# Kernel optimization log

Measured on AMD Instinct MI355X. Metric: run time of the kernel, lower is better.

## Reference

```python
import jax, jax.numpy as jnp
import numpy as np

N_NODES = 100000
N_EDGES = 800000
F_IN = 128
HID = 128
HEADS = 4
HEAD_DIM = HID // HEADS
LAYERS = 3
N_CLASSES = 40
NEG_SLOPE = 0.2
BN_EPS = 1e-5


def setup_inputs() -> dict:
    key = jax.random.key(0)
    ks = jax.random.split(key, 10)
    feat = jax.random.normal(ks[0], (N_NODES, F_IN), dtype=jnp.float32)
    src = jax.random.randint(ks[1], (N_EDGES,), 0, N_NODES, dtype=jnp.int32)
    dst = jax.random.randint(ks[2], (N_EDGES,), 0, N_NODES, dtype=jnp.int32)
    W_enc = jax.random.normal(ks[3], (F_IN, HID), dtype=jnp.float32) / np.sqrt(F_IN)
    b_enc = jnp.zeros((HID,), dtype=jnp.float32)
    Ws = jax.random.normal(ks[4], (LAYERS, HID, HID), dtype=jnp.float32) / np.sqrt(HID)
    attn_ls = jax.random.normal(ks[5], (LAYERS, HEADS, HEAD_DIM), dtype=jnp.float32) / np.sqrt(HEAD_DIM)
    attn_rs = jax.random.normal(ks[6], (LAYERS, HEADS, HEAD_DIM), dtype=jnp.float32) / np.sqrt(HEAD_DIM)
    biases = jnp.zeros((LAYERS, HID), dtype=jnp.float32)
    gammas = jnp.ones((LAYERS, HID), dtype=jnp.float32)
    betas = jnp.zeros((LAYERS, HID), dtype=jnp.float32)
    W_pred = jax.random.normal(ks[7], (HID, N_CLASSES), dtype=jnp.float32) / np.sqrt(HID)
    b_pred = jnp.zeros((N_CLASSES,), dtype=jnp.float32)
    return {"feat": feat, "src": src, "dst": dst, "W_enc": W_enc, "b_enc": b_enc,
            "Ws": Ws, "attn_ls": attn_ls, "attn_rs": attn_rs, "biases": biases,
            "gammas": gammas, "betas": betas, "W_pred": W_pred, "b_pred": b_pred}


def _gat_layer(h, src, dst, W, a_l, a_r, bias, n_nodes):
    # h: [N, HID] -> projected per-head features [N, H, D]
    hf = (h @ W).reshape(n_nodes, HEADS, HEAD_DIM)
    el = jnp.sum(hf * a_l, axis=-1)  # [N, H]
    er = jnp.sum(hf * a_r, axis=-1)  # [N, H]
    e = jax.nn.leaky_relu(el[src] + er[dst], NEG_SLOPE)  # [E, H]
    # edge softmax over incoming edges of each destination node
    m = jax.ops.segment_max(e, dst, num_segments=n_nodes)  # [N, H]
    ex = jnp.exp(e - m[dst])
    s = jax.ops.segment_sum(ex, dst, num_segments=n_nodes)  # [N, H]
    alpha = ex / s[dst]  # [E, H]
    msg = hf[src] * alpha[:, :, None]  # [E, H, D]
    out = jax.ops.segment_sum(msg, dst, num_segments=n_nodes)  # [N, H, D]
    return out.reshape(n_nodes, HEADS * HEAD_DIM) + bias


def _batchnorm(x, gamma, beta):
    mean = jnp.mean(x, axis=0)
    var = jnp.var(x, axis=0)
    return gamma * (x - mean) * jax.lax.rsqrt(var + BN_EPS) + beta


def reference(feat, src, dst, W_enc, b_enc, Ws, attn_ls, attn_rs, biases, gammas, betas, W_pred, b_pred):
    n_nodes = feat.shape[0]
    h = jax.nn.relu(feat @ W_enc + b_enc)
    h_last = None
    for i in range(Ws.shape[0]):
        h = _gat_layer(h, src, dst, Ws[i], attn_ls[i], attn_rs[i], biases[i], n_nodes)
        if h_last is not None:
            h = h + h_last
        h_last = h
        h = _batchnorm(h, gammas[i], betas[i])
        h = jax.nn.relu(h)
    return h @ W_pred + b_pred
```

## Files before the change

kernel.cpp:

```cpp
#include <hip/hip_runtime.h>

typedef __attribute__((ext_vector_type(8))) short short8;
typedef __attribute__((ext_vector_type(4))) float f32x4;

#define N_NODES 100000
#define N_EDGES 800000
#define NEG 0.2f
#define BN_EPS 1e-5f
#define AGG_GRID 2048

__device__ __forceinline__ ushort bf16b(float f) {
  unsigned u = __float_as_uint(f);
  return (ushort)((u + 0x7FFFu + ((u >> 16) & 1u)) >> 16);
}
__device__ __forceinline__ float bflo(unsigned u) { return __uint_as_float(u << 16); }
__device__ __forceinline__ float bfhi(unsigned u) { return __uint_as_float(u & 0xFFFF0000u); }

__global__ void k_hist(const int* __restrict__ dst, int* __restrict__ cnt, int e) {
  int i = blockIdx.x * blockDim.x + threadIdx.x;
  if (i < e) atomicAdd(&cnt[dst[i]], 1);
}

__global__ void k_scan1(const int* __restrict__ cnt, int* __restrict__ rowptr,
                        int* __restrict__ bsums, int n) {
  __shared__ int sm[256];
  int i = blockIdx.x * 256 + threadIdx.x;
  int v = (i < n) ? cnt[i] : 0;
  sm[threadIdx.x] = v;
  __syncthreads();
  for (int off = 1; off < 256; off <<= 1) {
    int t = (threadIdx.x >= off) ? sm[threadIdx.x - off] : 0;
    __syncthreads();
    sm[threadIdx.x] += t;
    __syncthreads();
  }
  if (i < n) rowptr[i + 1] = sm[threadIdx.x];
  if (threadIdx.x == 255) bsums[blockIdx.x] = sm[255];
}

__global__ void k_scan2(int* __restrict__ bsums, int nb) {
  __shared__ int sm[512];
  int v = (threadIdx.x < nb) ? bsums[threadIdx.x] : 0;
  sm[threadIdx.x] = v;
  __syncthreads();
  for (int off = 1; off < 512; off <<= 1) {
    int t = (threadIdx.x >= off) ? sm[threadIdx.x - off] : 0;
    __syncthreads();
    sm[threadIdx.x] += t;
    __syncthreads();
  }
  if (threadIdx.x < nb) bsums[threadIdx.x] = sm[threadIdx.x] - v;
}

__global__ void k_scan3(int* __restrict__ rowptr, const int* __restrict__ bsums,
                        int* __restrict__ cursor, int n) {
  int i = blockIdx.x * 256 + threadIdx.x;
  if (i < n) {
    int val = rowptr[i + 1] + bsums[blockIdx.x];
    rowptr[i + 1] = val;
    if (i + 1 < n) cursor[i + 1] = val;
  }
  if (i == 0) { rowptr[0] = 0; cursor[0] = 0; }
}

__global__ void k_scatter(const int* __restrict__ src, const int* __restrict__ dst,
                          int* __restrict__ cursor, int* __restrict__ ssort,
                          int* __restrict__ dsort, int e) {
  int i = blockIdx.x * blockDim.x + threadIdx.x;
  if (i < e) {
    int d = dst[i];
    int pos = atomicAdd(&cursor[d], 1);
    ssort[pos] = src[i];
    dsort[pos] = d;
  }
}

__global__ void k_packW(const float* __restrict__ W_enc, const float* __restrict__ Ws,
                        ushort* __restrict__ Wp) {
  int s = blockIdx.x * 256 + threadIdx.x;
  int wi = s >> 11, s2 = s & 2047;
  int kt = s2 >> 9, nb8 = (s2 >> 6) & 7, l = s2 & 63;
  const float* Wsrc = (wi == 0) ? W_enc : Ws + (size_t)(wi - 1) * 16384;
  int n = nb8 * 16 + (l & 15);
  int k0 = kt * 32 + (l >> 4) * 8;
  unsigned pk[4];
#pragma unroll
  for (int j = 0; j < 4; ++j) {
    ushort lo = bf16b(Wsrc[(size_t)(k0 + 2 * j) * 128 + n]);
    ushort hi = bf16b(Wsrc[(size_t)(k0 + 2 * j + 1) * 128 + n]);
    pk[j] = (unsigned)lo | ((unsigned)hi << 16);
  }
  *(uint4*)&Wp[(size_t)s * 8] = make_uint4(pk[0], pk[1], pk[2], pk[3]);
}

template <int MODE>
__global__ __launch_bounds__(256) void k_mgemm(
    const float* __restrict__ Af, const ushort* __restrict__ Ab,
    const ushort* __restrict__ Wp, const float* __restrict__ bias,
    const float* __restrict__ stats, const float* __restrict__ al,
    const float* __restrict__ ar, float* __restrict__ el, float* __restrict__ er,
    ushort* __restrict__ Cb) {
  __shared__ __align__(16) ushort Al[32 * 128];
  int tid = threadIdx.x;
  int lane = tid & 63, w = tid >> 6;
  int wr = w & 1, wc = w >> 1;
  int l15 = lane & 15, l4 = lane >> 4;
  int rb = blockIdx.x * 32;

  const uint4* wp4 = (const uint4*)Wp;
  short8 bfr[4][4];
#pragma unroll
  for (int kt = 0; kt < 4; ++kt) {
#pragma unroll
    for (int nb = 0; nb < 4; ++nb) {
      uint4 t = wp4[(size_t)((kt * 8 + wc * 4 + nb) * 64 + lane)];
      bfr[kt][nb] = *(short8*)&t;
    }
  }

  {
    int row = tid >> 3;
    int c16 = (tid & 7) * 16;
    int kc0 = (tid & 7) * 2;
    char* base = (char*)Al + row * 256;
    if (MODE == 1) {
      const uint4* srcp = (const uint4*)(Ab + (size_t)(rb + row) * 128 + c16);
      uint4 v0 = srcp[0], v1 = srcp[1];
      *(uint4*)(base + ((kc0 ^ (row & 7)) << 4)) = v0;
      *(uint4*)(base + (((kc0 + 1) ^ (row & 7)) << 4)) = v1;
    } else {
      const float4* srcp = (const float4*)(Af + (size_t)(rb + row) * 128 + c16);
      float4 f[4];
#pragma unroll
      for (int j = 0; j < 4; ++j) f[j] = srcp[j];
      if (MODE == 2) {
#pragma unroll
        for (int j = 0; j < 4; ++j) {
          float4 sc = *(const float4*)&stats[c16 + 4 * j];
          float4 sh = *(const float4*)&stats[128 + c16 + 4 * j];
          f[j].x = fmaxf(f[j].x * sc.x + sh.x, 0.f);
          f[j].y = fmaxf(f[j].y * sc.y + sh.y, 0.f);
          f[j].z = fmaxf(f[j].z * sc.z + sh.z, 0.f);
          f[j].w = fmaxf(f[j].w * sc.w + sh.w, 0.f);
        }
      }
      unsigned pk[8];
#pragma unroll
      for (int j = 0; j < 4; ++j) {
        pk[2 * j] = (unsigned)bf16b(f[j].x) | ((unsigned)bf16b(f[j].y) << 16);
        pk[2 * j + 1] = (unsigned)bf16b(f[j].z) | ((unsigned)bf16b(f[j].w) << 16);
      }
      *(uint4*)(base + ((kc0 ^ (row & 7)) << 4)) = make_uint4(pk[0], pk[1], pk[2], pk[3]);
      *(uint4*)(base + (((kc0 + 1) ^ (row & 7)) << 4)) = make_uint4(pk[4], pk[5], pk[6], pk[7]);
    }
  }
  __syncthreads();

  f32x4 acc[4];
#pragma unroll
  for (int nb = 0; nb < 4; ++nb) acc[nb] = (f32x4){0.f, 0.f, 0.f, 0.f};
  int arow = 16 * wr + l15;
  const char* abase = (const char*)Al + arow * 256;
  int sw = arow & 7;
#pragma unroll
  for (int kt = 0; kt < 4; ++kt) {
    short8 af = *(const short8*)(abase + (((kt * 4 + l4) ^ sw) << 4));
    acc[0] = __builtin_amdgcn_mfma_f32_16x16x32_bf16(af, bfr[kt][0], acc[0], 0, 0, 0);
    acc[1] = __builtin_amdgcn_mfma_f32_16x16x32_bf16(af, bfr[kt][1], acc[1], 0, 0, 0);
    acc[2] = __builtin_amdgcn_mfma_f32_16x16x32_bf16(af, bfr[kt][2], acc[2], 0, 0, 0);
    acc[3] = __builtin_amdgcn_mfma_f32_16x16x32_bf16(af, bfr[kt][3], acc[3], 0, 0, 0);
  }

  float alv0 = 0, alv1 = 0, alv2 = 0, alv3 = 0;
  float arv0 = 0, arv1 = 0, arv2 = 0, arv3 = 0;
  float bv0 = 0, bv1 = 0, bv2 = 0, bv3 = 0;
  if (MODE != 0) {
    alv0 = al[64 * wc + l15];      arv0 = ar[64 * wc + l15];
    alv1 = al[64 * wc + 16 + l15]; arv1 = ar[64 * wc + 16 + l15];
    alv2 = al[64 * wc + 32 + l15]; arv2 = ar[64 * wc + 32 + l15];
    alv3 = al[64 * wc + 48 + l15]; arv3 = ar[64 * wc + 48 + l15];
  } else {
    bv0 = bias[64 * wc + l15];      bv1 = bias[64 * wc + 16 + l15];
    bv2 = bias[64 * wc + 32 + l15]; bv3 = bias[64 * wc + 48 + l15];
  }
  int row0 = rb + 16 * wr + 4 * l4;
#pragma unroll
  for (int i = 0; i < 4; ++i) {
    int row = row0 + i;
    if (MODE != 0) {
      float pl0 = acc[0][i] * alv0 + acc[1][i] * alv1;
      float pr0 = acc[0][i] * arv0 + acc[1][i] * arv1;
      float pl1 = acc[2][i] * alv2 + acc[3][i] * alv3;
      float pr1 = acc[2][i] * arv2 + acc[3][i] * arv3;
#pragma unroll
      for (int o = 1; o < 16; o <<= 1) {
        pl0 += __shfl_xor(pl0, o); pr0 += __shfl_xor(pr0, o);
        pl1 += __shfl_xor(pl1, o); pr1 += __shfl_xor(pr1, o);
      }
      if (l15 == 0) {
        el[(size_t)row * 4 + 2 * wc] = pl0;     er[(size_t)row * 4 + 2 * wc] = pr0;
        el[(size_t)row * 4 + 2 * wc + 1] = pl1; er[(size_t)row * 4 + 2 * wc + 1] = pr1;
      }
    }
    float v0 = acc[0][i], v1 = acc[1][i], v2 = acc[2][i], v3 = acc[3][i];
    if (MODE == 0) {
      v0 = fmaxf(v0 + bv0, 0.f); v1 = fmaxf(v1 + bv1, 0.f);
      v2 = fmaxf(v2 + bv2, 0.f); v3 = fmaxf(v3 + bv3, 0.f);
    }
    size_t rbase = (size_t)row * 128 + 64 * wc + l15;
    Cb[rbase] = bf16b(v0);
    Cb[rbase + 16] = bf16b(v1);
    Cb[rbase + 32] = bf16b(v2);
    Cb[rbase + 48] = bf16b(v3);
  }
}

__global__ __launch_bounds__(256) void k_elmax1(const float* __restrict__ el,
                                                float4* __restrict__ part, int n) {
  int gid = blockIdx.x * 256 + threadIdx.x;
  float4 m = make_float4(-1e30f, -1e30f, -1e30f, -1e30f);
  for (int i = gid; i < n; i += 128 * 256) {
    float4 v = *(const float4*)&el[(size_t)4 * i];
    m.x = fmaxf(m.x, v.x); m.y = fmaxf(m.y, v.y);
    m.z = fmaxf(m.z, v.z); m.w = fmaxf(m.w, v.w);
  }
  __shared__ float4 sm[256];
  sm[threadIdx.x] = m;
  __syncthreads();
  for (int off = 128; off; off >>= 1) {
    if (threadIdx.x < off) {
      float4 o = sm[threadIdx.x + off];
      sm[threadIdx.x].x = fmaxf(sm[threadIdx.x].x, o.x);
      sm[threadIdx.x].y = fmaxf(sm[threadIdx.x].y, o.y);
      sm[threadIdx.x].z = fmaxf(sm[threadIdx.x].z, o.z);
      sm[threadIdx.x].w = fmaxf(sm[threadIdx.x].w, o.w);
    }
    __syncthreads();
  }
  if (threadIdx.x == 0) part[blockIdx.x] = sm[0];
}

__global__ void k_elmax2(const float4* __restrict__ part, float* __restrict__ elmax) {
  __shared__ float4 sm[128];
  int t = threadIdx.x;
  sm[t] = part[t];
  __syncthreads();
  for (int off = 64; off; off >>= 1) {
    if (t < off) {
      float4 o = sm[t + off];
      sm[t].x = fmaxf(sm[t].x, o.x);
      sm[t].y = fmaxf(sm[t].y, o.y);
      sm[t].z = fmaxf(sm[t].z, o.z);
      sm[t].w = fmaxf(sm[t].w, o.w);
    }
    __syncthreads();
  }
  if (t == 0) {
    elmax[0] = sm[0].x; elmax[1] = sm[0].y;
    elmax[2] = sm[0].z; elmax[3] = sm[0].w;
  }
}

__global__ __launch_bounds__(256) void k_edgew(
    const int* __restrict__ ssort, const int* __restrict__ dsort,
    const float* __restrict__ el, const float* __restrict__ er,
    const float* __restrict__ elmax, float4* __restrict__ wgt, int e) {
  int j = blockIdx.x * 256 + threadIdx.x;
  if (j >= e) return;
  int s = ssort[j], d = dsort[j];
  float4 elv = *(const float4*)&el[(size_t)4 * s];
  float4 erv = *(const float4*)&er[(size_t)4 * d];
  float m0 = elmax[0] + erv.x;
  float m1 = elmax[1] + erv.y;
  float m2 = elmax[2] + erv.z;
  float m3 = elmax[3] + erv.w;
  m0 = fmaxf(m0, NEG * m0); m1 = fmaxf(m1, NEG * m1);
  m2 = fmaxf(m2, NEG * m2); m3 = fmaxf(m3, NEG * m3);
  float e0 = elv.x + erv.x; e0 = fmaxf(e0, NEG * e0);
  float e1 = elv.y + erv.y; e1 = fmaxf(e1, NEG * e1);
  float e2 = elv.z + erv.z; e2 = fmaxf(e2, NEG * e2);
  float e3 = elv.w + erv.w; e3 = fmaxf(e3, NEG * e3);
  float4 wv;
  wv.x = __expf(e0 - m0); wv.y = __expf(e1 - m1);
  wv.z = __expf(e2 - m2); wv.w = __expf(e3 - m3);
  wgt[j] = wv;
}

__global__ __launch_bounds__(256, 8) void k_aggregate(
    const ushort* __restrict__ hf, const float4* __restrict__ wgt,
    const int* __restrict__ rowptr, const int* __restrict__ ssort,
    const float* __restrict__ bias, float* __restrict__ hpre,
    float* __restrict__ part, int n, int addres) {
  int tid = threadIdx.x;
  int w = tid >> 6, lane = tid & 63;
  int h = lane >> 4;
  int c0 = 2 * lane;
  float2 bb = *(const float2*)&bias[c0];
  float sbn0 = 0.f, sbn1 = 0.f, qbn0 = 0.f, qbn1 = 0.f;
  for (int wid = blockIdx.x * 4 + w; wid < n; wid += AGG_GRID * 4) {
    int beg = rowptr[wid], end = rowptr[wid + 1];
    float s0 = 0.f, a00 = 0.f, a10 = 0.f;
    float s1 = 0.f, a01 = 0.f, a11 = 0.f;
    float s2 = 0.f, a02 = 0.f, a12 = 0.f;
    float s3 = 0.f, a03 = 0.f, a13 = 0.f;
    int j = beg;
    int rem = (end - beg) & 3;
    for (int t = 0; t < rem; ++t, ++j) {
      int sA = ssort[j];
      float wA = ((const float*)(wgt + j))[h];
      unsigned hA = *(const unsigned*)(hf + (size_t)sA * 128 + c0);
      s0 += wA; a00 += wA * bflo(hA); a10 += wA * bfhi(hA);
    }
    for (; j < end; j += 4) {
      int sA = ssort[j], sB = ssort[j + 1], sC = ssort[j + 2], sD = ssort[j + 3];
      float wA = ((const float*)(wgt + j))[h];
      float wB = ((const float*)(wgt + j + 1))[h];
      float wC = ((const float*)(wgt + j + 2))[h];
      float wD = ((const float*)(wgt + j + 3))[h];
      unsigned hA = *(const unsigned*)(hf + (size_t)sA * 128 + c0);
      unsigned hB = *(const unsigned*)(hf + (size_t)sB * 128 + c0);
      unsigned hC = *(const unsigned*)(hf + (size_t)sC * 128 + c0);
      unsigned hD = *(const unsigned*)(hf + (size_t)sD * 128 + c0);
      s0 += wA; a00 += wA * bflo(hA); a10 += wA * bfhi(hA);
      s1 += wB; a01 += wB * bflo(hB); a11 += wB * bfhi(hB);
      s2 += wC; a02 += wC * bflo(hC); a12 += wC * bfhi(hC);
      s3 += wD; a03 += wD * bflo(hD); a13 += wD * bfhi(hD);
    }
    float s = (s0 + s1) + (s2 + s3);
    float inv = (end > beg) ? 1.f / s : 0.f;
    float a0 = ((a00 + a01) + (a02 + a03)) * inv;
    float a1 = ((a10 + a11) + (a12 + a13)) * inv;
    float r0 = 0.f, r1 = 0.f;
    if (addres) {
      float2 rr = *(const float2*)(hpre + (size_t)wid * 128 + c0);
      r0 = rr.x; r1 = rr.y;
    }
    float o0 = a0 + bb.x + r0, o1 = a1 + bb.y + r1;
    *(float2*)(hpre + (size_t)wid * 128 + c0) = make_float2(o0, o1);
    sbn0 += o0; qbn0 += o0 * o0;
    sbn1 += o1; qbn1 += o1 * o1;
  }
  __shared__ float red_s[4][128];
  __shared__ float red_q[4][128];
  red_s[w][c0] = sbn0; red_s[w][c0 + 1] = sbn1;
  red_q[w][c0] = qbn0; red_q[w][c0 + 1] = qbn1;
  __syncthreads();
  if (tid < 128)
    part[(size_t)blockIdx.x * 256 + tid] =
        (red_s[0][tid] + red_s[1][tid]) + (red_s[2][tid] + red_s[3][tid]);
  else if (tid < 256) {
    int c = tid - 128;
    part[(size_t)blockIdx.x * 256 + tid] =
        (red_q[0][c] + red_q[1][c]) + (red_q[2][c] + red_q[3][c]);
  }
}

__global__ __launch_bounds__(320) void k_pred(
    const float* __restrict__ A, const float* __restrict__ stats,
    const float* __restrict__ W, const float* __restrict__ bias,
    float* __restrict__ out, int n) {
  __shared__ float Wl[128 * 40];
  __shared__ float Xl[32 * 132];
  for (int i = threadIdx.x; i < 128 * 40; i += 320) Wl[i] = W[i];
  int cg = threadIdx.x % 10;
  int rg = threadIdx.x / 10;
  float4 bv = *(const float4*)&bias[4 * cg];
  for (int rb = blockIdx.x * 32; rb < n; rb += gridDim.x * 32) {
    __syncthreads();
    for (int idx = threadIdx.x; idx < 1024; idx += 320) {
      int r = idx >> 5, c = (idx & 31) * 4;
      float4 v = *(const float4*)&A[(size_t)(rb + r) * 128 + c];
      float4 sc = *(const float4*)&stats[c];
      float4 sh = *(const float4*)&stats[128 + c];
      v.x = fmaxf(v.x * sc.x + sh.x, 0.f);
      v.y = fmaxf(v.y * sc.y + sh.y, 0.f);
      v.z = fmaxf(v.z * sc.z + sh.z, 0.f);
      v.w = fmaxf(v.w * sc.w + sh.w, 0.f);
      *(float4*)&Xl[r * 132 + c] = v;
    }
    __syncthreads();
    float a0 = 0.f, a1 = 0.f, a2 = 0.f, a3 = 0.f;
#pragma unroll 4
    for (int k = 0; k < 128; ++k) {
      float x = Xl[rg * 132 + k];
      float4 w = *(float4*)&Wl[k * 40 + 4 * cg];
      a0 += x * w.x; a1 += x * w.y; a2 += x * w.z; a3 += x * w.w;
    }
    float4 o = make_float4(a0 + bv.x, a1 + bv.y, a2 + bv.z, a3 + bv.w);
    *(float4*)&out[(size_t)(rb + rg) * 40 + 4 * cg] = o;
  }
}

__global__ __launch_bounds__(256) void k_bnred(const float* __restrict__ part,
                                               float* __restrict__ colsum, int g) {
  int v = blockIdx.x;
  float acc = 0.f;
  for (int b = threadIdx.x; b < g; b += 256) acc += part[(size_t)b * 256 + v];
  __shared__ float sm[256];
  sm[threadIdx.x] = acc;
  __syncthreads();
  for (int off = 128; off; off >>= 1) {
    if (threadIdx.x < off) sm[threadIdx.x] += sm[threadIdx.x + off];
    __syncthreads();
  }
  if (threadIdx.x == 0) colsum[v] = sm[0];
}

__global__ void k_bnstat(const float* __restrict__ colsum, const float* __restrict__ gamma,
                         const float* __restrict__ beta, float* __restrict__ stats, int n) {
  int c = threadIdx.x;
  float mean = colsum[c] / n;
  float var = colsum[128 + c] / n - mean * mean;
  float rstd = rsqrtf(var + BN_EPS);
  float scale = gamma[c] * rstd;
  stats[c] = scale;
  stats[128 + c] = beta[c] - mean * scale;
}

extern "C" void kernel_launch(void* const* d_in, const int* in_sizes, int n_in,
                              void* d_out, int out_size, void* d_ws, size_t ws_size,
                              hipStream_t stream) {
  const float* feat   = (const float*)d_in[0];
  const int*   src    = (const int*)d_in[1];
  const int*   dst    = (const int*)d_in[2];
  const float* W_enc  = (const float*)d_in[3];
  const float* b_enc  = (const float*)d_in[4];
  const float* Ws     = (const float*)d_in[5];
  const float* a_ls   = (const float*)d_in[6];
  const float* a_rs   = (const float*)d_in[7];
  const float* biases = (const float*)d_in[8];
  const float* gammas = (const float*)d_in[9];
  const float* betas  = (const float*)d_in[10];
  const float* W_pred = (const float*)d_in[11];
  const float* b_pred = (const float*)d_in[12];
  float* out = (float*)d_out;

  char* p = (char*)d_ws;
  auto alloc = [&](size_t bytes) {
    char* q = p;
    p += (bytes + 255) & ~(size_t)255;
    return q;
  };
  ushort* h_bf  = (ushort*)alloc((size_t)N_NODES * 128 * 2);
  ushort* hf_bf = (ushort*)alloc((size_t)N_NODES * 128 * 2);
  float* hpre   = (float*)alloc((size_t)N_NODES * 128 * 4);
  float* el     = (float*)alloc((size_t)N_NODES * 4 * 4);
  float* er     = (float*)alloc((size_t)N_NODES * 4 * 4);
  float* part   = (float*)alloc((size_t)AGG_GRID * 256 * 4);
  float* colsum = (float*)alloc(256 * 4);
  float* stats  = (float*)alloc(256 * 4);
  ushort* Wpack = (ushort*)alloc((size_t)4 * 2048 * 16);
  float4* elpart= (float4*)alloc(128 * 16);
  float* elmax  = (float*)alloc(4 * 4);
  int* rowptr   = (int*)alloc((size_t)(N_NODES + 1) * 4);
  int* cursor   = (int*)alloc((size_t)N_NODES * 4);
  int* bsums    = (int*)alloc(512 * 4);
  int* ssort    = (int*)alloc((size_t)N_EDGES * 4);
  int* dsort    = (int*)alloc((size_t)N_EDGES * 4);
  float4* wgt   = (float4*)alloc((size_t)N_EDGES * 16);

  hipMemsetAsync(cursor, 0, (size_t)N_NODES * 4, stream);
  k_hist<<<(N_EDGES + 255) / 256, 256, 0, stream>>>(dst, cursor, N_EDGES);
  int nb = (N_NODES + 255) / 256;
  k_scan1<<<nb, 256, 0, stream>>>(cursor, rowptr, bsums, N_NODES);
  k_scan2<<<1, 512, 0, stream>>>(bsums, nb);
  k_scan3<<<nb, 256, 0, stream>>>(rowptr, bsums, cursor, N_NODES);
  k_scatter<<<(N_EDGES + 255) / 256, 256, 0, stream>>>(src, dst, cursor, ssort, dsort,
                                                       N_EDGES);

  k_packW<<<32, 256, 0, stream>>>(W_enc, Ws, Wpack);

  k_mgemm<0><<<3125, 256, 0, stream>>>(feat, nullptr, Wpack, b_enc, nullptr, nullptr,
                                       nullptr, nullptr, nullptr, h_bf);

  for (int L = 0; L < 3; ++L) {
    const float* al = a_ls + L * 128;
    const float* ar = a_rs + L * 128;
    const ushort* wp = Wpack + (size_t)(1 + L) * 16384;
    if (L == 0)
      k_mgemm<1><<<3125, 256, 0, stream>>>(nullptr, h_bf, wp, nullptr, nullptr, al, ar,
                                           el, er, hf_bf);
    else
      k_mgemm<2><<<3125, 256, 0, stream>>>(hpre, nullptr, wp, nullptr, stats, al, ar,
                                           el, er, hf_bf);
    k_elmax1<<<128, 256, 0, stream>>>(el, elpart, N_NODES);
    k_elmax2<<<1, 128, 0, stream>>>(elpart, elmax);
    k_edgew<<<(N_EDGES + 255) / 256, 256, 0, stream>>>(ssort, dsort, el, er, elmax,
                                                       wgt, N_EDGES);
    k_aggregate<<<AGG_GRID, 256, 0, stream>>>(hf_bf, wgt, rowptr, ssort,
                                              biases + L * 128, hpre, part, N_NODES,
                                              L > 0 ? 1 : 0);
    k_bnred<<<256, 256, 0, stream>>>(part, colsum, AGG_GRID);
    k_bnstat<<<1, 128, 0, stream>>>(colsum, gammas + L * 128, betas + L * 128, stats,
                                    N_NODES);
  }
  k_pred<<<1563, 320, 0, stream>>>(hpre, stats, W_pred, b_pred, out, N_NODES);
}
```

Measured before the change: 432.2 us.

## Store layer pre-activations in bf16 and interleave sorted src/dst indices

The per-layer aggregated output hpre (residual and BN input) is now stored as bf16 instead of fp32, which halves its read/write traffic in the aggregate, GEMM-prologue and prediction kernels. The sorted source and destination arrays are merged into one int2 array, so edge-weight computation issues a single load per edge. The cost is that the aggregate kernel now loads 8 bytes per edge where it only needs 4, and the residual path loses precision because it is accumulated from bf16 values across layers.

Result: faster. 419.2 us (-3.0%).

```diff
diff --git a/kernel.cpp b/kernel.cpp
--- a/kernel.cpp
+++ b/kernel.cpp
@@ -64,14 +64,12 @@
 }
 
 __global__ void k_scatter(const int* __restrict__ src, const int* __restrict__ dst,
-                          int* __restrict__ cursor, int* __restrict__ ssort,
-                          int* __restrict__ dsort, int e) {
+                          int* __restrict__ cursor, int2* __restrict__ esort, int e) {
   int i = blockIdx.x * blockDim.x + threadIdx.x;
   if (i < e) {
     int d = dst[i];
     int pos = atomicAdd(&cursor[d], 1);
-    ssort[pos] = src[i];
-    dsort[pos] = d;
+    esort[pos] = make_int2(src[i], d);
   }
 }
 
@@ -128,22 +126,35 @@
       uint4 v0 = srcp[0], v1 = srcp[1];
       *(uint4*)(base + ((kc0 ^ (row & 7)) << 4)) = v0;
       *(uint4*)(base + (((kc0 + 1) ^ (row & 7)) << 4)) = v1;
+    } else if (MODE == 2) {
+      const uint4* srcp = (const uint4*)(Ab + (size_t)(rb + row) * 128 + c16);
+      uint4 v0 = srcp[0], v1 = srcp[1];
+      unsigned pk[8];
+#pragma unroll
+      for (int j = 0; j < 4; ++j) {
+        unsigned wv = ((const unsigned*)&v0)[j];
+        float2 sc = *(const float2*)&stats[c16 + 2 * j];
+        float2 sh = *(const float2*)&stats[128 + c16 + 2 * j];
+        float x0 = fmaxf(bflo(wv) * sc.x + sh.x, 0.f);
+        float x1 = fmaxf(bfhi(wv) * sc.y + sh.y, 0.f);
+        pk[j] = (unsigned)bf16b(x0) | ((unsigned)bf16b(x1) << 16);
+      }
+#pragma unroll
+      for (int j = 0; j < 4; ++j) {
+        unsigned wv = ((const unsigned*)&v1)[j];
+        float2 sc = *(const float2*)&stats[c16 + 8 + 2 * j];
+        float2 sh = *(const float2*)&stats[128 + c16 + 8 + 2 * j];
+        float x0 = fmaxf(bflo(wv) * sc.x + sh.x, 0.f);
+        float x1 = fmaxf(bfhi(wv) * sc.y + sh.y, 0.f);
+        pk[4 + j] = (unsigned)bf16b(x0) | ((unsigned)bf16b(x1) << 16);
+      }
+      *(uint4*)(base + ((kc0 ^ (row & 7)) << 4)) = make_uint4(pk[0], pk[1], pk[2], pk[3]);
+      *(uint4*)(base + (((kc0 + 1) ^ (row & 7)) << 4)) = make_uint4(pk[4], pk[5], pk[6], pk[7]);
     } else {
       const float4* srcp = (const float4*)(Af + (size_t)(rb + row) * 128 + c16);
       float4 f[4];
 #pragma unroll
       for (int j = 0; j < 4; ++j) f[j] = srcp[j];
-      if (MODE == 2) {
-#pragma unroll
-        for (int j = 0; j < 4; ++j) {
-          float4 sc = *(const float4*)&stats[c16 + 4 * j];
-          float4 sh = *(const float4*)&stats[128 + c16 + 4 * j];
-          f[j].x = fmaxf(f[j].x * sc.x + sh.x, 0.f);
-          f[j].y = fmaxf(f[j].y * sc.y + sh.y, 0.f);
-          f[j].z = fmaxf(f[j].z * sc.z + sh.z, 0.f);
-          f[j].w = fmaxf(f[j].w * sc.w + sh.w, 0.f);
-        }
-      }
       unsigned pk[8];
 #pragma unroll
       for (int j = 0; j < 4; ++j) {
@@ -262,14 +273,14 @@
 }
 
 __global__ __launch_bounds__(256) void k_edgew(
-    const int* __restrict__ ssort, const int* __restrict__ dsort,
-    const float* __restrict__ el, const float* __restrict__ er,
-    const float* __restrict__ elmax, float4* __restrict__ wgt, int e) {
+    const int2* __restrict__ esort, const float* __restrict__ el,
+    const float* __restrict__ er, const float* __restrict__ elmax,
+    float4* __restrict__ wgt, int e) {
   int j = blockIdx.x * 256 + threadIdx.x;
   if (j >= e) return;
-  int s = ssort[j], d = dsort[j];
-  float4 elv = *(const float4*)&el[(size_t)4 * s];
-  float4 erv = *(const float4*)&er[(size_t)4 * d];
+  int2 sd = esort[j];
+  float4 elv = *(const float4*)&el[(size_t)4 * sd.x];
+  float4 erv = *(const float4*)&er[(size_t)4 * sd.y];
   float m0 = elmax[0] + erv.x;
   float m1 = elmax[1] + erv.y;
   float m2 = elmax[2] + erv.z;
@@ -288,8 +299,8 @@
 
 __global__ __launch_bounds__(256, 8) void k_aggregate(
     const ushort* __restrict__ hf, const float4* __restrict__ wgt,
-    const int* __restrict__ rowptr, const int* __restrict__ ssort,
-    const float* __restrict__ bias, float* __restrict__ hpre,
+    const int* __restrict__ rowptr, const int2* __restrict__ esort,
+    const float* __restrict__ bias, ushort* __restrict__ hpre,
     float* __restrict__ part, int n, int addres) {
   int tid = threadIdx.x;
   int w = tid >> 6, lane = tid & 63;
@@ -306,13 +317,13 @@
     int j = beg;
     int rem = (end - beg) & 3;
     for (int t = 0; t < rem; ++t, ++j) {
-      int sA = ssort[j];
+      int sA = esort[j].x;
       float wA = ((const float*)(wgt + j))[h];
       unsigned hA = *(const unsigned*)(hf + (size_t)sA * 128 + c0);
       s0 += wA; a00 += wA * bflo(hA); a10 += wA * bfhi(hA);
     }
     for (; j < end; j += 4) {
-      int sA = ssort[j], sB = ssort[j + 1], sC = ssort[j + 2], sD = ssort[j + 3];
+      int sA = esort[j].x, sB = esort[j + 1].x, sC = esort[j + 2].x, sD = esort[j + 3].x;
       float wA = ((const float*)(wgt + j))[h];
       float wB = ((const float*)(wgt + j + 1))[h];
       float wC = ((const float*)(wgt + j + 2))[h];
@@ -332,11 +343,12 @@
     float a1 = ((a10 + a11) + (a12 + a13)) * inv;
     float r0 = 0.f, r1 = 0.f;
     if (addres) {
-      float2 rr = *(const float2*)(hpre + (size_t)wid * 128 + c0);
-      r0 = rr.x; r1 = rr.y;
+      unsigned rr = *(const unsigned*)(hpre + (size_t)wid * 128 + c0);
+      r0 = bflo(rr); r1 = bfhi(rr);
     }
     float o0 = a0 + bb.x + r0, o1 = a1 + bb.y + r1;
-    *(float2*)(hpre + (size_t)wid * 128 + c0) = make_float2(o0, o1);
+    *(unsigned*)(hpre + (size_t)wid * 128 + c0) =
+        (unsigned)bf16b(o0) | ((unsigned)bf16b(o1) << 16);
     sbn0 += o0; qbn0 += o0 * o0;
     sbn1 += o1; qbn1 += o1 * o1;
   }
@@ -356,7 +368,7 @@
 }
 
 __global__ __launch_bounds__(320) void k_pred(
-    const float* __restrict__ A, const float* __restrict__ stats,
+    const ushort* __restrict__ A, const float* __restrict__ stats,
     const float* __restrict__ W, const float* __restrict__ bias,
     float* __restrict__ out, int n) {
   __shared__ float Wl[128 * 40];
@@ -369,14 +381,14 @@
     __syncthreads();
     for (int idx = threadIdx.x; idx < 1024; idx += 320) {
       int r = idx >> 5, c = (idx & 31) * 4;
-      float4 v = *(const float4*)&A[(size_t)(rb + r) * 128 + c];
+      uint2 v = *(const uint2*)(A + (size_t)(rb + r) * 128 + c);
       float4 sc = *(const float4*)&stats[c];
       float4 sh = *(const float4*)&stats[128 + c];
-      v.x = fmaxf(v.x * sc.x + sh.x, 0.f);
-      v.y = fmaxf(v.y * sc.y + sh.y, 0.f);
-      v.z = fmaxf(v.z * sc.z + sh.z, 0.f);
-      v.w = fmaxf(v.w * sc.w + sh.w, 0.f);
-      *(float4*)&Xl[r * 132 + c] = v;
+      float x0 = fmaxf(bflo(v.x) * sc.x + sh.x, 0.f);
+      float x1 = fmaxf(bfhi(v.x) * sc.y + sh.y, 0.f);
+      float x2 = fmaxf(bflo(v.y) * sc.z + sh.z, 0.f);
+      float x3 = fmaxf(bfhi(v.y) * sc.w + sh.w, 0.f);
+      *(float4*)&Xl[r * 132 + c] = make_float4(x0, x1, x2, x3);
     }
     __syncthreads();
     float a0 = 0.f, a1 = 0.f, a2 = 0.f, a3 = 0.f;
@@ -443,7 +455,7 @@
   };
   ushort* h_bf  = (ushort*)alloc((size_t)N_NODES * 128 * 2);
   ushort* hf_bf = (ushort*)alloc((size_t)N_NODES * 128 * 2);
-  float* hpre   = (float*)alloc((size_t)N_NODES * 128 * 4);
+  ushort* hpre  = (ushort*)alloc((size_t)N_NODES * 128 * 2);
   float* el     = (float*)alloc((size_t)N_NODES * 4 * 4);
   float* er     = (float*)alloc((size_t)N_NODES * 4 * 4);
   float* part   = (float*)alloc((size_t)AGG_GRID * 256 * 4);
@@ -455,8 +467,7 @@
   int* rowptr   = (int*)alloc((size_t)(N_NODES + 1) * 4);
   int* cursor   = (int*)alloc((size_t)N_NODES * 4);
   int* bsums    = (int*)alloc(512 * 4);
-  int* ssort    = (int*)alloc((size_t)N_EDGES * 4);
-  int* dsort    = (int*)alloc((size_t)N_EDGES * 4);
+  int2* esort   = (int2*)alloc((size_t)N_EDGES * 8);
   float4* wgt   = (float4*)alloc((size_t)N_EDGES * 16);
 
   hipMemsetAsync(cursor, 0, (size_t)N_NODES * 4, stream);
@@ -465,8 +476,7 @@
   k_scan1<<<nb, 256, 0, stream>>>(cursor, rowptr, bsums, N_NODES);
   k_scan2<<<1, 512, 0, stream>>>(bsums, nb);
   k_scan3<<<nb, 256, 0, stream>>>(rowptr, bsums, cursor, N_NODES);
-  k_scatter<<<(N_EDGES + 255) / 256, 256, 0, stream>>>(src, dst, cursor, ssort, dsort,
-                                                       N_EDGES);
+  k_scatter<<<(N_EDGES + 255) / 256, 256, 0, stream>>>(src, dst, cursor, esort, N_EDGES);
 
   k_packW<<<32, 256, 0, stream>>>(W_enc, Ws, Wpack);
 
@@ -481,13 +491,13 @@
       k_mgemm<1><<<3125, 256, 0, stream>>>(nullptr, h_bf, wp, nullptr, nullptr, al, ar,
                                            el, er, hf_bf);
     else
-      k_mgemm<2><<<3125, 256, 0, stream>>>(hpre, nullptr, wp, nullptr, stats, al, ar,
+      k_mgemm<2><<<3125, 256, 0, stream>>>(nullptr, hpre, wp, nullptr, stats, al, ar,
                                            el, er, hf_bf);
     k_elmax1<<<128, 256, 0, stream>>>(el, elpart, N_NODES);
     k_elmax2<<<1, 128, 0, stream>>>(elpart, elmax);
-    k_edgew<<<(N_EDGES + 255) / 256, 256, 0, stream>>>(ssort, dsort, el, er, elmax,
-                                                       wgt, N_EDGES);
-    k_aggregate<<<AGG_GRID, 256, 0, stream>>>(hf_bf, wgt, rowptr, ssort,
+    k_edgew<<<(N_EDGES + 255) / 256, 256, 0, stream>>>(esort, el, er, elmax, wgt,
+                                                       N_EDGES);
+    k_aggregate<<<AGG_GRID, 256, 0, stream>>>(hf_bf, wgt, rowptr, esort,
                                               biases + L * 128, hpre, part, N_NODES,
                                               L > 0 ? 1 : 0);
     k_bnred<<<256, 256, 0, stream>>>(part, colsum, AGG_GRID);
```
